# Performance work log

Measured on AMD Instinct MI355X. Metric: run time of the kernel, lower is better.

Reference implementation:

```python
import jax, jax.numpy as jnp
import numpy as np

N, E, D, R = 50000, 800000, 128, 200


def setup_inputs() -> dict:
    key = jax.random.key(0)
    ks = jax.random.split(key, 8)
    h = jax.random.normal(ks[0], (N, D), jnp.float32)
    emb_rel = jax.random.normal(ks[1], (R, D), jnp.float32)
    loop_weight = jax.random.normal(ks[2], (D, D), jnp.float32) * 0.05
    attn_fc_w = jax.random.normal(ks[3], (D, 3 * D), jnp.float32) * 0.05  # Linear(3D,D) weight [D,3D]
    attn_fc2_w = jax.random.normal(ks[4], (1, D), jnp.float32) * 0.05     # Linear(D,1) weight [1,D]
    src = jax.random.randint(ks[5], (E,), 0, N)
    dst = jax.random.randint(ks[6], (E,), 0, N)
    etype = jax.random.randint(ks[7], (E,), 0, R)
    return {"h": h, "emb_rel": emb_rel, "loop_weight": loop_weight,
            "attn_fc_w": attn_fc_w, "attn_fc2_w": attn_fc2_w,
            "src": src, "dst": dst, "etype": etype}


def reference(h, emb_rel, loop_weight, attn_fc_w, attn_fc2_w, src, dst, etype):
    num_nodes = h.shape[0]
    # attn_fc(concat([h_src, h_dst, rel])) == h_src@Ws.T + h_dst@Wd.T + rel@Wr.T
    # (avoids materializing the [E, 3D] concat)
    Ws, Wd, Wr = jnp.split(attn_fc_w, 3, axis=1)  # each [D, D]
    hs = h[src]  # [E, D] gathered source features
    a = hs @ Ws.T + h[dst] @ Wd.T + emb_rel[etype] @ Wr.T  # [E, D]
    e = jax.nn.leaky_relu((a @ attn_fc2_w.T)[:, 0], 0.01)  # [E] edge logits
    # segment softmax over destination node (stable)
    m = jax.ops.segment_max(e, dst, num_segments=num_nodes)
    w = jnp.exp(e - m[dst])
    denom = jax.ops.segment_sum(w, dst, num_segments=num_nodes)
    alpha = w / denom[dst]  # [E]
    # weighted scatter-sum of source features into destination nodes
    agg = jax.ops.segment_sum(alpha[:, None] * hs, dst, num_segments=num_nodes)
    # DGL update_all leaves zero-in-degree nodes' feature unchanged
    deg = jax.ops.segment_sum(jnp.ones_like(e), dst, num_segments=num_nodes)
    agg = jnp.where(deg[:, None] > 0, agg, h)
    # self-loop message
    return agg + h @ loop_weight
```

## Files before the change

kernel.cpp:

```cpp
#include <hip/hip_runtime.h>

#define D 128
#define TD 384

__global__ void k_prep(const float* __restrict__ A, const float* __restrict__ v,
                       float* __restrict__ p) {
  __shared__ float vs[D];
  int t = threadIdx.x;
  if (t < D) vs[t] = v[t];
  __syncthreads();
  float acc = 0.f;
#pragma unroll 8
  for (int i = 0; i < D; ++i) acc += vs[i] * A[i * TD + t];
  p[t] = acc;
}

__global__ void k_scores_hist(const float* __restrict__ h, const float* __restrict__ emb,
                              const float* __restrict__ p, const int* __restrict__ dst,
                              float* __restrict__ ss, float* __restrict__ sd,
                              float* __restrict__ sr, int* __restrict__ cnt,
                              int N, int R, int E, int nbScore) {
  int t = threadIdx.x;
  if ((int)blockIdx.x < nbScore) {
    __shared__ float pl[TD];
    pl[t] = p[t];
    if (t < TD - 256) pl[256 + t] = p[256 + t];
    __syncthreads();
    int w = blockIdx.x * 4 + (t >> 6);
    int l = t & 63;
    if (w < N) {
      float x0 = h[(size_t)w * D + l];
      float x1 = h[(size_t)w * D + 64 + l];
      float a = x0 * pl[l] + x1 * pl[64 + l];
      float b = x0 * pl[128 + l] + x1 * pl[192 + l];
#pragma unroll
      for (int o = 32; o; o >>= 1) { a += __shfl_xor(a, o); b += __shfl_xor(b, o); }
      if (l == 0) { ss[w] = a; sd[w] = b; }
    } else if (w < N + R) {
      int r = w - N;
      float x0 = emb[(size_t)r * D + l];
      float x1 = emb[(size_t)r * D + 64 + l];
      float c = x0 * pl[256 + l] + x1 * pl[320 + l];
#pragma unroll
      for (int o = 32; o; o >>= 1) c += __shfl_xor(c, o);
      if (l == 0) sr[r] = c;
    }
  } else {
    int i = (blockIdx.x - nbScore) * 256 + t;
    int stride = (gridDim.x - nbScore) * 256;
    for (; i < E; i += stride) atomicAdd(&cnt[dst[i]], 1);
  }
}

__global__ void k_scan1(int* __restrict__ cnt, int* __restrict__ bsum, int N) {
  __shared__ int wsum[16];
  int t = threadIdx.x, lane = t & 63, wid = t >> 6;
  int i = blockIdx.x * 1024 + t;
  int v = (i < N) ? cnt[i] : 0;
  int x = v;
#pragma unroll
  for (int o = 1; o < 64; o <<= 1) {
    int y = __shfl_up(x, o);
    if (lane >= o) x += y;
  }
  if (lane == 63) wsum[wid] = x;
  __syncthreads();
  if (t < 16) {
    int y = wsum[t];
#pragma unroll
    for (int o = 1; o < 16; o <<= 1) {
      int z = __shfl_up(y, o);
      if (t >= o) y += z;
    }
    wsum[t] = y;
  }
  __syncthreads();
  int woff = wid ? wsum[wid - 1] : 0;
  if (i < N) cnt[i] = woff + x - v;
  if (t == 0) bsum[blockIdx.x] = wsum[15];
}

__global__ void k_scan2(int* __restrict__ bsum, int nsb) {
  int l = threadIdx.x;
  int v = (l < nsb) ? bsum[l] : 0;
  int x = v;
#pragma unroll
  for (int o = 1; o < 64; o <<= 1) {
    int y = __shfl_up(x, o);
    if (l >= o) x += y;
  }
  if (l < nsb) bsum[l] = x - v;
}

__global__ void k_scan3(const int* __restrict__ bsum, int* __restrict__ cnt,
                        int* __restrict__ cur, int N, int E) {
  int i = blockIdx.x * 1024 + threadIdx.x;
  if (i < N) {
    int v = cnt[i] + bsum[blockIdx.x];
    cnt[i] = v;
    cur[i] = v;
  }
  if (i == 0) cnt[N] = E;
}

__global__ void k_edge(const int* __restrict__ src, const int* __restrict__ dst,
                       const int* __restrict__ et, const float* __restrict__ ss,
                       const float* __restrict__ sd, const float* __restrict__ sr,
                       int* __restrict__ cur, float* __restrict__ esort,
                       int* __restrict__ ssort, int E) {
  int i = blockIdx.x * blockDim.x + threadIdx.x;
  if (i >= E) return;
  int s = src[i], d = dst[i], r = et[i];
  float e = ss[s] + sd[d] + sr[r];
  e = (e > 0.f) ? e : 0.01f * e;
  int pos = atomicAdd(&cur[d], 1);
  esort[pos] = e;
  ssort[pos] = s;
}

__global__ __launch_bounds__(256) void k_agg(const float* __restrict__ h,
                                             const int* __restrict__ off,
                                             const float* __restrict__ esort,
                                             const int* __restrict__ ssort,
                                             float* __restrict__ out, int N) {
  int n = blockIdx.x;
  int t = threadIdx.x;
  int start = off[n], deg = off[n + 1] - start;
  int qc = t & 31;
  int slot = t >> 5;
  if (deg == 0) {
    if (slot == 0)
      ((float4*)(out + (size_t)n * D))[qc] = ((const float4*)(h + (size_t)n * D))[qc];
    return;
  }
  __shared__ float4 part[8][32];
  __shared__ float dpart[8];
  __shared__ float mred[4];

  float m = -3.4e38f;
  for (int i = t; i < deg; i += 256) m = fmaxf(m, esort[start + i]);
#pragma unroll
  for (int o = 32; o; o >>= 1) m = fmaxf(m, __shfl_xor(m, o));
  if ((t & 63) == 0) mred[t >> 6] = m;
  __syncthreads();
  m = fmaxf(fmaxf(mred[0], mred[1]), fmaxf(mred[2], mred[3]));

  float4 acc = {0.f, 0.f, 0.f, 0.f};
  float wpriv = 0.f;
  for (int i = slot; i < deg; i += 8) {
    float w = __expf(esort[start + i] - m);
    int s = ssort[start + i];
    float4 hv = ((const float4*)(h + (size_t)s * D))[qc];
    acc.x = fmaf(w, hv.x, acc.x);
    acc.y = fmaf(w, hv.y, acc.y);
    acc.z = fmaf(w, hv.z, acc.z);
    acc.w = fmaf(w, hv.w, acc.w);
    wpriv += w;
  }
  part[slot][qc] = acc;
  if (qc == 0) dpart[slot] = wpriv;
  __syncthreads();
  if (slot == 0) {
    float4 s4 = part[0][qc];
#pragma unroll
    for (int s2 = 1; s2 < 8; ++s2) {
      float4 p4 = part[s2][qc];
      s4.x += p4.x; s4.y += p4.y; s4.z += p4.z; s4.w += p4.w;
    }
    float denom = ((dpart[0] + dpart[1]) + (dpart[2] + dpart[3])) +
                  ((dpart[4] + dpart[5]) + (dpart[6] + dpart[7]));
    float inv = 1.f / denom;
    float4 r;
    r.x = s4.x * inv; r.y = s4.y * inv; r.z = s4.z * inv; r.w = s4.w * inv;
    ((float4*)(out + (size_t)n * D))[qc] = r;
  }
}

__global__ __launch_bounds__(128, 2) void k_final(const float* __restrict__ h,
                                                  const float* __restrict__ lw,
                                                  float* __restrict__ out, int N) {
  int j = threadIdx.x;
  float w[D];
#pragma unroll
  for (int k = 0; k < D; ++k) w[k] = lw[(size_t)k * D + j];
#pragma unroll
  for (int k = 0; k < D; ++k) asm volatile("" : "+v"(w[k]));

  int stride = gridDim.x;
  for (int n = blockIdx.x; n < N; n += 2 * stride) {
    int n2 = n + stride;
    const float4* __restrict__ ra = (const float4*)(h + (size_t)n * D);
    float a0 = 0.f, a1 = 0.f, a2 = 0.f, a3 = 0.f;
    float b0 = 0.f, b1 = 0.f, b2 = 0.f, b3 = 0.f;
    if (n2 < N) {
      const float4* __restrict__ rb = (const float4*)(h + (size_t)n2 * D);
#pragma unroll
      for (int q = 0; q < D / 4; ++q) {
        float4 va = ra[q];
        float4 vb = rb[q];
        a0 = fmaf(va.x, w[4 * q + 0], a0);
        a1 = fmaf(va.y, w[4 * q + 1], a1);
        a2 = fmaf(va.z, w[4 * q + 2], a2);
        a3 = fmaf(va.w, w[4 * q + 3], a3);
        b0 = fmaf(vb.x, w[4 * q + 0], b0);
        b1 = fmaf(vb.y, w[4 * q + 1], b1);
        b2 = fmaf(vb.z, w[4 * q + 2], b2);
        b3 = fmaf(vb.w, w[4 * q + 3], b3);
      }
      out[(size_t)n * D + j] += (a0 + a1) + (a2 + a3);
      out[(size_t)n2 * D + j] += (b0 + b1) + (b2 + b3);
    } else {
#pragma unroll
      for (int q = 0; q < D / 4; ++q) {
        float4 va = ra[q];
        a0 = fmaf(va.x, w[4 * q + 0], a0);
        a1 = fmaf(va.y, w[4 * q + 1], a1);
        a2 = fmaf(va.z, w[4 * q + 2], a2);
        a3 = fmaf(va.w, w[4 * q + 3], a3);
      }
      out[(size_t)n * D + j] += (a0 + a1) + (a2 + a3);
    }
  }
}

extern "C" void kernel_launch(void* const* d_in, const int* in_sizes, int n_in,
                              void* d_out, int out_size, void* d_ws, size_t ws_size,
                              hipStream_t stream) {
  const float* h   = (const float*)d_in[0];
  const float* emb = (const float*)d_in[1];
  const float* lw  = (const float*)d_in[2];
  const float* afw = (const float*)d_in[3];
  const float* af2 = (const float*)d_in[4];
  const int* src = (const int*)d_in[5];
  const int* dst = (const int*)d_in[6];
  const int* et  = (const int*)d_in[7];
  int N = in_sizes[0] / D;
  int R = in_sizes[1] / D;
  int E = in_sizes[5];
  float* out = (float*)d_out;

  char* ws = (char*)d_ws;
  size_t o = 0;
  auto alloc = [&](size_t bytes) -> void* {
    void* pp = ws + o;
    o = (o + bytes + 255) & ~(size_t)255;
    return pp;
  };
  float* p     = (float*)alloc((size_t)TD * 4);
  float* ss    = (float*)alloc((size_t)N * 4);
  float* sd    = (float*)alloc((size_t)N * 4);
  float* srel  = (float*)alloc((size_t)R * 4);
  int*   cnt   = (int*)  alloc((size_t)(N + 1) * 4);
  int*   cur   = (int*)  alloc((size_t)N * 4);
  int*   bsum  = (int*)  alloc((size_t)64 * 4);
  float* esort = (float*)alloc((size_t)E * 4);
  int*   ssort = (int*)  alloc((size_t)E * 4);

  int nsb = (N + 1023) / 1024;

  hipMemsetAsync(cnt, 0, (size_t)(N + 1) * 4, stream);
  k_prep<<<1, TD, 0, stream>>>(afw, af2, p);
  int nbScore = (N + R + 3) / 4;
  int nbHist = 2048;
  k_scores_hist<<<nbScore + nbHist, 256, 0, stream>>>(h, emb, p, dst, ss, sd, srel,
                                                      cnt, N, R, E, nbScore);
  k_scan1<<<nsb, 1024, 0, stream>>>(cnt, bsum, N);
  k_scan2<<<1, 64, 0, stream>>>(bsum, nsb);
  k_scan3<<<nsb, 1024, 0, stream>>>(bsum, cnt, cur, N, E);
  k_edge<<<(E + 255) / 256, 256, 0, stream>>>(src, dst, et, ss, sd, srel, cur,
                                              esort, ssort, E);
  k_agg<<<N, 256, 0, stream>>>(h, cnt, esort, ssort, out, N);
  k_final<<<1024, 128, 0, stream>>>(h, lw, out, N);
}
```

Measured before the change: 356.1 us.

## Precompute self-loop matmul into workspace and fuse addition into aggregation kernel

```diff
diff --git a/kernel.cpp b/kernel.cpp
--- a/kernel.cpp
+++ b/kernel.cpp
@@ -13,6 +13,47 @@
 #pragma unroll 8
   for (int i = 0; i < D; ++i) acc += vs[i] * A[i * TD + t];
   p[t] = acc;
+}
+
+__global__ __launch_bounds__(256) void k_sl(const float* __restrict__ h,
+                                            const float* __restrict__ lw,
+                                            float* __restrict__ sl, int N) {
+  int t = threadIdx.x;
+  int j = t & 127;
+  int half = t >> 7;
+  float w[64];
+#pragma unroll
+  for (int kk = 0; kk < 64; ++kk)
+    w[kk] = lw[(size_t)(half * 64 + kk) * D + j];
+  __shared__ float red[4][D];
+  int stride4 = gridDim.x * 4;
+  for (int base = blockIdx.x * 4; base < N; base += stride4) {
+    float acc[4] = {0.f, 0.f, 0.f, 0.f};
+#pragma unroll
+    for (int u = 0; u < 4; ++u) {
+      int n = base + u;
+      if (n < N) {
+        const float* __restrict__ hr = h + (size_t)n * D + half * 64;
+        float a = 0.f;
+#pragma unroll
+        for (int kk = 0; kk < 64; ++kk) a = fmaf(hr[kk], w[kk], a);
+        acc[u] = a;
+      }
+    }
+    __syncthreads();
+    if (half == 1) {
+#pragma unroll
+      for (int u = 0; u < 4; ++u) red[u][j] = acc[u];
+    }
+    __syncthreads();
+    if (half == 0) {
+#pragma unroll
+      for (int u = 0; u < 4; ++u) {
+        int n = base + u;
+        if (n < N) sl[(size_t)n * D + j] = acc[u] + red[u][j];
+      }
+    }
+  }
 }
 
 __global__ void k_scores_hist(const float* __restrict__ h, const float* __restrict__ emb,
@@ -122,6 +163,7 @@
                                              const int* __restrict__ off,
                                              const float* __restrict__ esort,
                                              const int* __restrict__ ssort,
+                                             const float* __restrict__ sl,
                                              float* __restrict__ out, int N) {
   int n = blockIdx.x;
   int t = threadIdx.x;
@@ -129,8 +171,12 @@
   int qc = t & 31;
   int slot = t >> 5;
   if (deg == 0) {
-    if (slot == 0)
-      ((float4*)(out + (size_t)n * D))[qc] = ((const float4*)(h + (size_t)n * D))[qc];
+    if (slot == 0) {
+      float4 hv = ((const float4*)(h + (size_t)n * D))[qc];
+      float4 sv = ((const float4*)(sl + (size_t)n * D))[qc];
+      hv.x += sv.x; hv.y += sv.y; hv.z += sv.z; hv.w += sv.w;
+      ((float4*)(out + (size_t)n * D))[qc] = hv;
+    }
     return;
   }
   __shared__ float4 part[8][32];
@@ -170,56 +216,13 @@
     float denom = ((dpart[0] + dpart[1]) + (dpart[2] + dpart[3])) +
                   ((dpart[4] + dpart[5]) + (dpart[6] + dpart[7]));
     float inv = 1.f / denom;
+    float4 sv = ((const float4*)(sl + (size_t)n * D))[qc];
     float4 r;
-    r.x = s4.x * inv; r.y = s4.y * inv; r.z = s4.z * inv; r.w = s4.w * inv;
+    r.x = fmaf(s4.x, inv, sv.x);
+    r.y = fmaf(s4.y, inv, sv.y);
+    r.z = fmaf(s4.z, inv, sv.z);
+    r.w = fmaf(s4.w, inv, sv.w);
     ((float4*)(out + (size_t)n * D))[qc] = r;
-  }
-}
-
-__global__ __launch_bounds__(128, 2) void k_final(const float* __restrict__ h,
-                                                  const float* __restrict__ lw,
-                                                  float* __restrict__ out, int N) {
-  int j = threadIdx.x;
-  float w[D];
-#pragma unroll
-  for (int k = 0; k < D; ++k) w[k] = lw[(size_t)k * D + j];
-#pragma unroll
-  for (int k = 0; k < D; ++k) asm volatile("" : "+v"(w[k]));
-
-  int stride = gridDim.x;
-  for (int n = blockIdx.x; n < N; n += 2 * stride) {
-    int n2 = n + stride;
-    const float4* __restrict__ ra = (const float4*)(h + (size_t)n * D);
-    float a0 = 0.f, a1 = 0.f, a2 = 0.f, a3 = 0.f;
-    float b0 = 0.f, b1 = 0.f, b2 = 0.f, b3 = 0.f;
-    if (n2 < N) {
-      const float4* __restrict__ rb = (const float4*)(h + (size_t)n2 * D);
-#pragma unroll
-      for (int q = 0; q < D / 4; ++q) {
-        float4 va = ra[q];
-        float4 vb = rb[q];
-        a0 = fmaf(va.x, w[4 * q + 0], a0);
-        a1 = fmaf(va.y, w[4 * q + 1], a1);
-        a2 = fmaf(va.z, w[4 * q + 2], a2);
-        a3 = fmaf(va.w, w[4 * q + 3], a3);
-        b0 = fmaf(vb.x, w[4 * q + 0], b0);
-        b1 = fmaf(vb.y, w[4 * q + 1], b1);
-        b2 = fmaf(vb.z, w[4 * q + 2], b2);
-        b3 = fmaf(vb.w, w[4 * q + 3], b3);
-      }
-      out[(size_t)n * D + j] += (a0 + a1) + (a2 + a3);
-      out[(size_t)n2 * D + j] += (b0 + b1) + (b2 + b3);
-    } else {
-#pragma unroll
-      for (int q = 0; q < D / 4; ++q) {
-        float4 va = ra[q];
-        a0 = fmaf(va.x, w[4 * q + 0], a0);
-        a1 = fmaf(va.y, w[4 * q + 1], a1);
-        a2 = fmaf(va.z, w[4 * q + 2], a2);
-        a3 = fmaf(va.w, w[4 * q + 3], a3);
-      }
-      out[(size_t)n * D + j] += (a0 + a1) + (a2 + a3);
-    }
   }
 }
 
@@ -255,11 +258,13 @@
   int*   bsum  = (int*)  alloc((size_t)64 * 4);
   float* esort = (float*)alloc((size_t)E * 4);
   int*   ssort = (int*)  alloc((size_t)E * 4);
+  float* slws  = (float*)alloc((size_t)N * D * 4);
 
   int nsb = (N + 1023) / 1024;
 
   hipMemsetAsync(cnt, 0, (size_t)(N + 1) * 4, stream);
   k_prep<<<1, TD, 0, stream>>>(afw, af2, p);
+  k_sl<<<1024, 256, 0, stream>>>(h, lw, slws, N);
   int nbScore = (N + R + 3) / 4;
   int nbHist = 2048;
   k_scores_hist<<<nbScore + nbHist, 256, 0, stream>>>(h, emb, p, dst, ss, sd, srel,
@@ -269,6 +274,5 @@
   k_scan3<<<nsb, 1024, 0, stream>>>(bsum, cnt, cur, N, E);
   k_edge<<<(E + 255) / 256, 256, 0, stream>>>(src, dst, et, ss, sd, srel, cur,
                                               esort, ssort, E);
-  k_agg<<<N, 256, 0, stream>>>(h, cnt, esort, ssort, out, N);
-  k_final<<<1024, 128, 0, stream>>>(h, lw, out, N);
-}
+  k_agg<<<N, 256, 0, stream>>>(h, cnt, esort, ssort, slws, out, N);
+}
```

Result: slower. 378.0 us (+6.2%).
